# Optimization experiments

Hardware: AMD Instinct MI355X
Metric: run time of the kernel (lower is better)

## Reference

```python
import jax, jax.numpy as jnp
import numpy as np

NUM_HEADS = 16
KEY_DIM = 64
VALUE_DIM = 64
D_MODEL = 1024
NEG_INF = -1e10


def setup_inputs() -> dict:
    key = jax.random.key(0)
    ks = jax.random.split(key, 8)
    B, T, S, D = 4, 2048, 2048, D_MODEL
    w_scale = 1.0 / np.sqrt(D)  # keep logits well-scaled
    inp = {
        'query': jax.random.normal(ks[0], (B, T, D), jnp.float32),
        'key':   jax.random.normal(ks[1], (B, S, D), jnp.float32),
        'value': jax.random.normal(ks[2], (B, S, D), jnp.float32),
        'Wq': jax.random.normal(ks[3], (D, NUM_HEADS * KEY_DIM), jnp.float32) * w_scale,
        'bq': jnp.zeros((NUM_HEADS * KEY_DIM,), jnp.float32),
        'Wk': jax.random.normal(ks[4], (D, NUM_HEADS * KEY_DIM), jnp.float32) * w_scale,
        'bk': jnp.zeros((NUM_HEADS * KEY_DIM,), jnp.float32),
        'Wv': jax.random.normal(ks[5], (D, NUM_HEADS * VALUE_DIM), jnp.float32) * w_scale,
        'bv': jnp.zeros((NUM_HEADS * VALUE_DIM,), jnp.float32),
        'Wo': jax.random.normal(ks[6], (NUM_HEADS * VALUE_DIM, D), jnp.float32) * w_scale,
        'bo': jnp.zeros((D,), jnp.float32),
    }
    return inp


def reference(query, key, value, Wq, bq, Wk, bk, Wv, bv, Wo, bo):
    B, T, _ = query.shape
    S = key.shape[1]
    H, Dk, Dv = NUM_HEADS, KEY_DIM, VALUE_DIM
    # QKV projections -> (B, T/S, H, D_head)
    q = (query @ Wq + bq).reshape(B, T, H, Dk)
    k = (key @ Wk + bk).reshape(B, S, H, Dk)
    v = (value @ Wv + bv).reshape(B, S, H, Dv)
    # scaled dot-product scores: (B, H, T, S)
    q = q * (1.0 / jnp.sqrt(jnp.asarray(Dk, q.dtype)))
    scores = jnp.einsum('bthd,bshd->bhts', q, k)
    # causal mask [1,1,T,S], additive -1e10 on masked positions (as in source)
    causal = jnp.tril(jnp.ones((T, S), scores.dtype))
    scores = scores + NEG_INF * (1.0 - causal)
    attn = jax.nn.softmax(scores, axis=-1)
    # dropout rate = 0.0 -> identity
    ctx = jnp.einsum('bhts,bshd->bthd', attn, v).reshape(B, T, H * Dv)
    out = ctx @ Wo + bo
    return out
```

## Files before the change

kernel.cpp:

```cpp
#include <hip/hip_runtime.h>
#include <cstdint>

#define DEV static __device__ __forceinline__

typedef unsigned short u16;
typedef unsigned int u32;
using short8 = __attribute__((ext_vector_type(8))) short;
using f32x2  = __attribute__((ext_vector_type(2))) float;
using f32x4  = __attribute__((ext_vector_type(4))) float;
using f32x8  = __attribute__((ext_vector_type(8))) float;
using f32x16 = __attribute__((ext_vector_type(16))) float;
using u32x4  = __attribute__((ext_vector_type(4))) unsigned int;

constexpr int Bz = 4, Tz = 2048, Dz = 1024, Hz = 16;
constexpr float QSCALE = 0.125f * 1.4426950408889634f;

DEV u16 f2bf(float x) {
  union { float f; u32 u; } c; c.f = x;
  u32 u = c.u;
  return (u16)((u + 0x7FFFu + ((u >> 16) & 1u)) >> 16);
}

DEV u32 cvtpk(float a, float b) {
  u32 r;
  asm("v_cvt_pk_bf16_f32 %0, %1, %2" : "=v"(r) : "v"(a), "v"(b));
  return r;
}

DEV void gload16(const void* g, void* l) {
  __builtin_amdgcn_global_load_lds(
      (const __attribute__((address_space(1))) void*)g,
      (__attribute__((address_space(3))) void*)l, 16, 0, 0);
}

__global__ __launch_bounds__(256) void cvt_kernel(
    const float* __restrict__ Xq, const float* __restrict__ Xk,
    const float* __restrict__ Xv, u16* __restrict__ Yq,
    u16* __restrict__ Yk, u16* __restrict__ Yv) {
  int z = blockIdx.y;
  const float* X = z == 0 ? Xq : z == 1 ? Xk : Xv;
  u16* Y         = z == 0 ? Yq : z == 1 ? Yk : Yv;
  size_t i = (size_t)blockIdx.x * 256 + threadIdx.x;
  float4 a = ((const float4*)X)[i * 2];
  float4 b = ((const float4*)X)[i * 2 + 1];
  uint4 o;
  o.x = cvtpk(a.x, a.y); o.y = cvtpk(a.z, a.w);
  o.z = cvtpk(b.x, b.y); o.w = cvtpk(b.z, b.w);
  ((uint4*)Y)[i] = o;
}

__global__ void wt_kernel(const float* __restrict__ W0, const float* __restrict__ W1,
                          const float* __restrict__ W2, const float* __restrict__ W3,
                          u16* __restrict__ T0, u16* __restrict__ T1,
                          u16* __restrict__ T2, u16* __restrict__ T3) {
  __shared__ float tile[32][33];
  int z = blockIdx.z;
  const float* W = z == 0 ? W0 : z == 1 ? W1 : z == 2 ? W2 : W3;
  u16* WT = z == 0 ? T0 : z == 1 ? T1 : z == 2 ? T2 : T3;
  int n0 = blockIdx.x * 32, k0 = blockIdx.y * 32;
  int tx = threadIdx.x & 31, ty = threadIdx.x >> 5;
  #pragma unroll
  for (int i = 0; i < 32; i += 8)
    tile[ty + i][tx] = W[(size_t)(k0 + ty + i) * Dz + n0 + tx];
  __syncthreads();
  #pragma unroll
  for (int i = 0; i < 32; i += 8)
    WT[(size_t)(n0 + ty + i) * Dz + k0 + tx] = f2bf(tile[tx][ty + i]);
}

template <int EPI>
DEV void gemm_core(const u16* __restrict__ A, const u16* __restrict__ WT,
                   const float* __restrict__ bias, void* __restrict__ Cptr,
                   float scale, int n0, int m0, char* L)
{
  const int tid = threadIdx.x;
  const int lane = tid & 63, wid = tid >> 6;
  const int g = lane >> 4, l15 = lane & 15;
  const int wm = (wid >> 1) * 64, wn = (wid & 1) * 64;

  f32x4 acc[4][4] = {};

  const int srow = tid >> 3, scolb = (tid & 7) * 16;
  const int scbs = scolb ^ ((srow & 7) << 4);

  for (int step = 0; step < 16; ++step) {
    const int k0 = step * 64;
    #pragma unroll
    for (int i = 0; i < 4; ++i) {
      int row = srow + i * 32;
      gload16(A + (size_t)(m0 + row) * Dz + k0 + (scbs >> 1),
              L + (tid + i * 256) * 16);
    }
    #pragma unroll
    for (int i = 0; i < 4; ++i) {
      int row = srow + i * 32;
      gload16(WT + (size_t)(n0 + row) * Dz + k0 + (scbs >> 1),
              L + 16384 + (tid + i * 256) * 16);
    }
    __syncthreads();

    #pragma unroll
    for (int kc = 0; kc < 2; ++kc) {
      short8 af[4], bfv[4];
      #pragma unroll
      for (int mt = 0; mt < 4; ++mt) {
        int row = wm + mt * 16 + l15;
        af[mt] = *(const short8*)(L + row * 128 + ((kc * 64 + g * 16) ^ ((row & 7) << 4)));
      }
      #pragma unroll
      for (int nt = 0; nt < 4; ++nt) {
        int row = wn + nt * 16 + l15;
        bfv[nt] = *(const short8*)(L + 16384 + row * 128 + ((kc * 64 + g * 16) ^ ((row & 7) << 4)));
      }
      #pragma unroll
      for (int mt = 0; mt < 4; ++mt)
        #pragma unroll
        for (int nt = 0; nt < 4; ++nt)
          acc[mt][nt] = __builtin_amdgcn_mfma_f32_16x16x32_bf16(af[mt], bfv[nt], acc[mt][nt], 0, 0, 0);
    }
    __syncthreads();
  }

  if (EPI == 0) {
    u16* C = (u16*)Cptr;
    #pragma unroll
    for (int nt = 0; nt < 4; ++nt) {
      int n = n0 + wn + nt * 16 + l15;
      float bv = bias[n];
      #pragma unroll
      for (int mt = 0; mt < 4; ++mt)
        #pragma unroll
        for (int r = 0; r < 4; ++r) {
          int m = m0 + wm + mt * 16 + g * 4 + r;
          C[(size_t)m * Dz + n] = f2bf((acc[mt][nt][r] + bv) * scale);
        }
    }
  } else if (EPI == 1) {
    float* C = (float*)Cptr;
    #pragma unroll
    for (int nt = 0; nt < 4; ++nt) {
      int n = n0 + wn + nt * 16 + l15;
      float bv = bias[n];
      #pragma unroll
      for (int mt = 0; mt < 4; ++mt)
        #pragma unroll
        for (int r = 0; r < 4; ++r) {
          int m = m0 + wm + mt * 16 + g * 4 + r;
          C[(size_t)m * Dz + n] = acc[mt][nt][r] + bv;
        }
    }
  } else {
    u16* VT = (u16*)Cptr;
    #pragma unroll
    for (int nt = 0; nt < 4; ++nt) {
      int nrel = wn + nt * 16 + l15;
      float bv = bias[n0 + nrel];
      int swz = (nrel & 7) << 4;
      #pragma unroll
      for (int mt = 0; mt < 4; ++mt) {
        int mrel0 = wm + mt * 16 + g * 4;
        uint2 p = make_uint2(cvtpk(acc[mt][nt][0] + bv, acc[mt][nt][1] + bv),
                             cvtpk(acc[mt][nt][2] + bv, acc[mt][nt][3] + bv));
        *(uint2*)(L + nrel * 256 + ((mrel0 * 2) ^ swz)) = p;
      }
    }
    __syncthreads();
    int n = tid & 127, strip = tid >> 7;
    int nn = n0 + n;
    int h = nn >> 6, dv = nn & 63;
    int b = m0 >> 11;
    int tb = m0 & 2047;
    int swz = (n & 7) << 4;
    u16* dst = VT + (((size_t)(b * Hz + h) * 64 + dv) * Tz) + tb + strip * 64;
    #pragma unroll
    for (int c = 0; c < 8; ++c) {
      uint4 v = *(const uint4*)(L + n * 256 + ((strip * 128 + c * 16) ^ swz));
      *(uint4*)(dst + c * 8) = v;
    }
  }
}

__global__ __launch_bounds__(256, 4) void qkv_kernel(
    const u16* __restrict__ Aq, const u16* __restrict__ Ak, const u16* __restrict__ Av,
    const u16* __restrict__ Wq, const u16* __restrict__ Wk, const u16* __restrict__ Wv,
    const float* __restrict__ bq, const float* __restrict__ bk, const float* __restrict__ bv,
    u16* __restrict__ oq, u16* __restrict__ ok, u16* __restrict__ ovt)
{
  __shared__ char lds[32768];
  int z = blockIdx.z;
  int n0 = blockIdx.y * 128, m0 = blockIdx.x * 128;
  if (z == 0)
    gemm_core<0>(Aq, Wq, bq, oq, QSCALE, n0, m0, lds);
  else if (z == 1)
    gemm_core<0>(Ak, Wk, bk, ok, 1.0f, n0, m0, lds);
  else
    gemm_core<2>(Av, Wv, bv, ovt, 1.0f, n0, m0, lds);
}

__global__ __launch_bounds__(256, 4) void out_gemm_kernel(
    const u16* __restrict__ A, const u16* __restrict__ WT,
    const float* __restrict__ bias, float* __restrict__ C)
{
  __shared__ char lds[32768];
  gemm_core<1>(A, WT, bias, C, 1.0f, blockIdx.y * 128, blockIdx.x * 128, lds);
}

DEV short8 mk_pb(float p0, float p1, float p2, float p3,
                 float p4, float p5, float p6, float p7) {
  u32 x0 = cvtpk(p0, p1), y0 = cvtpk(p4, p5);
  u32 x1 = cvtpk(p2, p3), y1 = cvtpk(p6, p7);
  asm("v_permlane32_swap_b32 %0, %1" : "+v"(x0), "+v"(y0));
  asm("v_permlane32_swap_b32 %0, %1" : "+v"(x1), "+v"(y1));
  u32x4 w = {x0, x1, y0, y1};
  return __builtin_bit_cast(short8, w);
}

DEV float vsum16(f32x16 a, f32x16 b) {
  f32x16 s = a + b;
  f32x8 s8 = __builtin_shufflevector(s, s, 0, 1, 2, 3, 4, 5, 6, 7) +
             __builtin_shufflevector(s, s, 8, 9, 10, 11, 12, 13, 14, 15);
  f32x4 s4 = __builtin_shufflevector(s8, s8, 0, 1, 2, 3) +
             __builtin_shufflevector(s8, s8, 4, 5, 6, 7);
  f32x2 s2 = __builtin_shufflevector(s4, s4, 0, 1) +
             __builtin_shufflevector(s4, s4, 2, 3);
  return s2[0] + s2[1];
}

__global__ __launch_bounds__(512) void attn_kernel(
    const u16* __restrict__ Q, const u16* __restrict__ K,
    const u16* __restrict__ VT, u16* __restrict__ CTX)
{
  __shared__ char lds[65536];

  const int tid = threadIdx.x;
  const int lane = tid & 63, wave = tid >> 6;
  const int s = wave >> 2, w4 = wave & 3;
  const int l31 = lane & 31, hi = lane >> 5;
  const int pr = blockIdx.y;
  const int bh = blockIdx.x;
  const int b = bh >> 4, h = bh & 15;

  const u16* qb  = Q  + (size_t)b * Tz * Dz + h * 64;
  const u16* kb  = K  + (size_t)b * Tz * Dz + h * 64;
  const u16* vtb = VT + (size_t)bh * 64 * Tz;

  #pragma unroll 1
  for (int half = 0; half < 2; ++half) {
    const int j = half ? (15 - pr) : pr;
    const int t0 = j * 128;
    const int nsteps = j + 1;
    const int wq0 = t0 + w4 * 32;
    const int qg = wq0 + l31, wqhi = wq0 + 31;
    const int tbase = s * nsteps;

    auto stage = [&](int buf, int step) {
      #pragma unroll
      for (int i = 0; i < 4; ++i) {
        int c = tid + i * 512;
        int sc = c >> 10, r = c & 1023;
        int tn = r >> 9, e = r & 511;
        int row = e >> 3, colb = (e & 7) * 16;
        int cbs = colb ^ ((row & 7) << 4);
        int kv0 = (sc * nsteps + step) * 64;
        char* dst = lds + ((sc * 2 + buf) << 14) + (tn << 13) + e * 16;
        if (tn == 0)
          gload16(kb + (size_t)(kv0 + row) * Dz + (cbs >> 1), dst);
        else
          gload16(vtb + (size_t)row * Tz + kv0 + (cbs >> 1), dst);
      }
    };

    stage(0, 0);

    short8 qf[4];
    #pragma unroll
    for (int kc = 0; kc < 4; ++kc)
      qf[kc] = *(const short8*)(qb + (size_t)qg * Dz + kc * 16 + hi * 8);

    f32x16 o0 = {}, o1 = {};
    float l_run = 0.f;

    __syncthreads();

    int cur = 0;
    for (int step = 0; step < nsteps; ++step) {
      if (step + 1 < nsteps) stage(cur ^ 1, step + 1);
      const int kv0 = (tbase + step) * 64;

      if (kv0 <= wqhi) {
        const char* Kl = lds + ((s * 2 + cur) << 14);
        const char* Vl = Kl + 8192;
        const int swz = (l31 & 7) << 4;

        f32x16 s0 = {}, s1 = {};
        __builtin_amdgcn_s_setprio(1);
        #pragma unroll
        for (int kc = 0; kc < 4; ++kc) {
          int cb = (kc * 32 + hi * 16) ^ swz;
          short8 kf0 = *(const short8*)(Kl + l31 * 128 + cb);
          short8 kf1 = *(const short8*)(Kl + (32 + l31) * 128 + cb);
          s0 = __builtin_amdgcn_mfma_f32_32x32x16_bf16(kf0, qf[kc], s0, 0, 0, 0);
          s1 = __builtin_amdgcn_mfma_f32_32x32x16_bf16(kf1, qf[kc], s1, 0, 0, 0);
        }
        __builtin_amdgcn_s_setprio(0);

        if (kv0 + 63 > wq0) {
          #pragma unroll
          for (int r = 0; r < 16; ++r) {
            int kg = kv0 + (r & 3) + 8 * (r >> 2) + 4 * hi;
            if (kg > qg)      s0[r] = -3.0e38f;
            if (kg + 32 > qg) s1[r] = -3.0e38f;
          }
        }

        #pragma unroll
        for (int r = 0; r < 16; ++r) {
          s0[r] = __builtin_amdgcn_exp2f(s0[r]);
          s1[r] = __builtin_amdgcn_exp2f(s1[r]);
        }
        float psum = vsum16(s0, s1);
        psum += __shfl_xor(psum, 32);
        l_run += psum;

        short8 pb0 = mk_pb(s0[0], s0[1], s0[2],  s0[3],  s0[4],  s0[5],  s0[6],  s0[7]);
        short8 pb1 = mk_pb(s0[8], s0[9], s0[10], s0[11], s0[12], s0[13], s0[14], s0[15]);
        short8 pb2 = mk_pb(s1[0], s1[1], s1[2],  s1[3],  s1[4],  s1[5],  s1[6],  s1[7]);
        short8 pb3 = mk_pb(s1[8], s1[9], s1[10], s1[11], s1[12], s1[13], s1[14], s1[15]);

        __builtin_amdgcn_s_setprio(1);
        #pragma unroll
        for (int kc = 0; kc < 4; ++kc) {
          int cb = (kc * 32 + hi * 16) ^ swz;
          short8 vf0 = *(const short8*)(Vl + l31 * 128 + cb);
          short8 vf1 = *(const short8*)(Vl + (32 + l31) * 128 + cb);
          short8 pbk = (kc == 0) ? pb0 : (kc == 1) ? pb1 : (kc == 2) ? pb2 : pb3;
          o0 = __builtin_amdgcn_mfma_f32_32x32x16_bf16(vf0, pbk, o0, 0, 0, 0);
          o1 = __builtin_amdgcn_mfma_f32_32x32x16_bf16(vf1, pbk, o1, 0, 0, 0);
        }
        __builtin_amdgcn_s_setprio(0);
      }

      __syncthreads();
      cur ^= 1;
    }

    if (s == 1) {
      char* P = lds + w4 * 9216 + lane * 144;
      #pragma unroll
      for (int r2 = 0; r2 < 4; ++r2) {
        f32x4 a = {o0[4*r2], o0[4*r2+1], o0[4*r2+2], o0[4*r2+3]};
        *(f32x4*)(P + r2 * 16) = a;
        f32x4 c = {o1[4*r2], o1[4*r2+1], o1[4*r2+2], o1[4*r2+3]};
        *(f32x4*)(P + 64 + r2 * 16) = c;
      }
      *(float*)(P + 128) = l_run;
    }
    __syncthreads();
    if (s == 0) {
      const char* P = lds + w4 * 9216 + lane * 144;
      float l1 = *(const float*)(P + 128);
      float inv = 1.0f / (l_run + l1);

      u16* cp = CTX + ((size_t)(b * Tz + qg)) * Dz + h * 64;
      #pragma unroll
      for (int rq = 0; rq < 4; ++rq) {
        f32x4 p0 = *(const f32x4*)(P + rq * 16);
        f32x4 p1 = *(const f32x4*)(P + 64 + rq * 16);
        int dv0 = 8 * rq + 4 * hi;
        float a0 = (o0[rq*4+0] + p0[0]) * inv;
        float a1 = (o0[rq*4+1] + p0[1]) * inv;
        float a2 = (o0[rq*4+2] + p0[2]) * inv;
        float a3 = (o0[rq*4+3] + p0[3]) * inv;
        *(uint2*)(cp + dv0) = make_uint2(cvtpk(a0, a1), cvtpk(a2, a3));
        float c0 = (o1[rq*4+0] + p1[0]) * inv;
        float c1 = (o1[rq*4+1] + p1[1]) * inv;
        float c2 = (o1[rq*4+2] + p1[2]) * inv;
        float c3 = (o1[rq*4+3] + p1[3]) * inv;
        *(uint2*)(cp + 32 + dv0) = make_uint2(cvtpk(c0, c1), cvtpk(c2, c3));
      }
    }
    __syncthreads();
  }
}

extern "C" void kernel_launch(void* const* d_in, const int* in_sizes, int n_in,
                              void* d_out, int out_size, void* d_ws, size_t ws_size,
                              hipStream_t stream) {
  (void)in_sizes; (void)n_in; (void)out_size; (void)ws_size;
  const float* query = (const float*)d_in[0];
  const float* key   = (const float*)d_in[1];
  const float* value = (const float*)d_in[2];
  const float* Wq = (const float*)d_in[3];
  const float* bq = (const float*)d_in[4];
  const float* Wk = (const float*)d_in[5];
  const float* bk = (const float*)d_in[6];
  const float* Wv = (const float*)d_in[7];
  const float* bv = (const float*)d_in[8];
  const float* Wo = (const float*)d_in[9];
  const float* bo = (const float*)d_in[10];

  char* ws = (char*)d_ws;
  const size_t SZ_ACT = (size_t)Bz * Tz * Dz * sizeof(u16);
  const size_t SZ_W = (size_t)Dz * Dz * sizeof(u16);
  u16* qw  = (u16*)(ws);
  u16* kw  = (u16*)(ws + SZ_ACT);
  u16* vw  = (u16*)(ws + 2 * SZ_ACT);
  u16* vtw = (u16*)(ws + 3 * SZ_ACT);
  u16* qx  = vw;
  u16* cw  = vw;
  u16* wqt = (u16*)(ws + 4 * SZ_ACT);
  u16* wkt = (u16*)(ws + 4 * SZ_ACT + SZ_W);
  u16* wvt = (u16*)(ws + 4 * SZ_ACT + 2 * SZ_W);
  u16* wot = (u16*)(ws + 4 * SZ_ACT + 3 * SZ_W);
  u16* kx = (u16*)d_out;
  u16* vx = (u16*)d_out + (size_t)Bz * Tz * Dz;

  const int CVTG = (Bz * Tz * Dz) / (256 * 8);
  cvt_kernel<<<dim3(CVTG, 3), 256, 0, stream>>>(query, key, value, qx, kx, vx);

  wt_kernel<<<dim3(32, 32, 4), 256, 0, stream>>>(Wq, Wk, Wv, Wo, wqt, wkt, wvt, wot);

  qkv_kernel<<<dim3(64, 8, 3), 256, 0, stream>>>(qx, kx, vx,
                                                 wqt, wkt, wvt,
                                                 bq, bk, bv,
                                                 qw, kw, vtw);

  attn_kernel<<<dim3(Bz * Hz, 8), 512, 0, stream>>>(qw, kw, vtw, cw);

  out_gemm_kernel<<<dim3(64, 8), 256, 0, stream>>>(cw, wot, bo, (float*)d_out);
}
```

Before: 171.0 us.

## Fuse fp32-to-bf16 activation conversion into QKV GEMM A-tile loads

Removes the separate conversion kernel and has the QKV GEMM load fp32 activations directly into LDS (with a wider swizzle), converting to bf16 when reading fragments. This drops one full read-write pass over the three activation tensors and a kernel launch. In exchange, each GEMM block reads twice as many A bytes per tile, across all 8 N-tile blocks. LDS use grows to 48KB and occupancy drops from 4 to 3 blocks, and conversion ALU work moves into the MFMA inner loop.

```diff
diff --git a/kernel.cpp b/kernel.cpp
--- a/kernel.cpp
+++ b/kernel.cpp
@@ -31,22 +31,6 @@
   __builtin_amdgcn_global_load_lds(
       (const __attribute__((address_space(1))) void*)g,
       (__attribute__((address_space(3))) void*)l, 16, 0, 0);
-}
-
-__global__ __launch_bounds__(256) void cvt_kernel(
-    const float* __restrict__ Xq, const float* __restrict__ Xk,
-    const float* __restrict__ Xv, u16* __restrict__ Yq,
-    u16* __restrict__ Yk, u16* __restrict__ Yv) {
-  int z = blockIdx.y;
-  const float* X = z == 0 ? Xq : z == 1 ? Xk : Xv;
-  u16* Y         = z == 0 ? Yq : z == 1 ? Yk : Yv;
-  size_t i = (size_t)blockIdx.x * 256 + threadIdx.x;
-  float4 a = ((const float4*)X)[i * 2];
-  float4 b = ((const float4*)X)[i * 2 + 1];
-  uint4 o;
-  o.x = cvtpk(a.x, a.y); o.y = cvtpk(a.z, a.w);
-  o.z = cvtpk(b.x, b.y); o.w = cvtpk(b.z, b.w);
-  ((uint4*)Y)[i] = o;
 }
 
 __global__ void wt_kernel(const float* __restrict__ W0, const float* __restrict__ W1,
@@ -68,11 +52,13 @@
     WT[(size_t)(n0 + ty + i) * Dz + k0 + tx] = f2bf(tile[tx][ty + i]);
 }
 
-template <int EPI>
-DEV void gemm_core(const u16* __restrict__ A, const u16* __restrict__ WT,
+template <int AFP32, int EPI>
+DEV void gemm_core(const void* __restrict__ Aptr, const u16* __restrict__ WT,
                    const float* __restrict__ bias, void* __restrict__ Cptr,
                    float scale, int n0, int m0, char* L)
 {
+  constexpr int BOFF = AFP32 ? 32768 : 16384;
+
   const int tid = threadIdx.x;
   const int lane = tid & 63, wid = tid >> 6;
   const int g = lane >> 4, l15 = lane & 15;
@@ -82,20 +68,33 @@
 
   const int srow = tid >> 3, scolb = (tid & 7) * 16;
   const int scbs = scolb ^ ((srow & 7) << 4);
+  const int frow = tid >> 4, fcolb = (tid & 15) * 16;
+  const int fcbs = fcolb ^ ((frow & 7) << 5);
 
   for (int step = 0; step < 16; ++step) {
     const int k0 = step * 64;
-    #pragma unroll
-    for (int i = 0; i < 4; ++i) {
-      int row = srow + i * 32;
-      gload16(A + (size_t)(m0 + row) * Dz + k0 + (scbs >> 1),
-              L + (tid + i * 256) * 16);
+    if (AFP32) {
+      const float* A = (const float*)Aptr;
+      #pragma unroll
+      for (int i = 0; i < 8; ++i) {
+        int row = frow + i * 16;
+        gload16(A + (size_t)(m0 + row) * Dz + k0 + (fcbs >> 2),
+                L + (tid + i * 256) * 16);
+      }
+    } else {
+      const u16* A = (const u16*)Aptr;
+      #pragma unroll
+      for (int i = 0; i < 4; ++i) {
+        int row = srow + i * 32;
+        gload16(A + (size_t)(m0 + row) * Dz + k0 + (scbs >> 1),
+                L + (tid + i * 256) * 16);
+      }
     }
     #pragma unroll
     for (int i = 0; i < 4; ++i) {
       int row = srow + i * 32;
       gload16(WT + (size_t)(n0 + row) * Dz + k0 + (scbs >> 1),
-              L + 16384 + (tid + i * 256) * 16);
+              L + BOFF + (tid + i * 256) * 16);
     }
     __syncthreads();
 
@@ -105,12 +104,21 @@
       #pragma unroll
       for (int mt = 0; mt < 4; ++mt) {
         int row = wm + mt * 16 + l15;
-        af[mt] = *(const short8*)(L + row * 128 + ((kc * 64 + g * 16) ^ ((row & 7) << 4)));
+        if (AFP32) {
+          const char* p = L + row * 256 + ((kc * 128 + g * 32) ^ ((row & 7) << 5));
+          f32x4 lo = *(const f32x4*)p;
+          f32x4 hi = *(const f32x4*)(p + 16);
+          u32x4 w = {cvtpk(lo[0], lo[1]), cvtpk(lo[2], lo[3]),
+                     cvtpk(hi[0], hi[1]), cvtpk(hi[2], hi[3])};
+          af[mt] = __builtin_bit_cast(short8, w);
+        } else {
+          af[mt] = *(const short8*)(L + row * 128 + ((kc * 64 + g * 16) ^ ((row & 7) << 4)));
+        }
       }
       #pragma unroll
       for (int nt = 0; nt < 4; ++nt) {
         int row = wn + nt * 16 + l15;
-        bfv[nt] = *(const short8*)(L + 16384 + row * 128 + ((kc * 64 + g * 16) ^ ((row & 7) << 4)));
+        bfv[nt] = *(const short8*)(L + BOFF + row * 128 + ((kc * 64 + g * 16) ^ ((row & 7) << 4)));
       }
       #pragma unroll
       for (int mt = 0; mt < 4; ++mt)
@@ -180,21 +188,21 @@
   }
 }
 
-__global__ __launch_bounds__(256, 4) void qkv_kernel(
-    const u16* __restrict__ Aq, const u16* __restrict__ Ak, const u16* __restrict__ Av,
+__global__ __launch_bounds__(256, 3) void qkv_kernel(
+    const float* __restrict__ Aq, const float* __restrict__ Ak, const float* __restrict__ Av,
     const u16* __restrict__ Wq, const u16* __restrict__ Wk, const u16* __restrict__ Wv,
     const float* __restrict__ bq, const float* __restrict__ bk, const float* __restrict__ bv,
     u16* __restrict__ oq, u16* __restrict__ ok, u16* __restrict__ ovt)
 {
-  __shared__ char lds[32768];
+  __shared__ char lds[49152];
   int z = blockIdx.z;
   int n0 = blockIdx.y * 128, m0 = blockIdx.x * 128;
   if (z == 0)
-    gemm_core<0>(Aq, Wq, bq, oq, QSCALE, n0, m0, lds);
+    gemm_core<1, 0>(Aq, Wq, bq, oq, QSCALE, n0, m0, lds);
   else if (z == 1)
-    gemm_core<0>(Ak, Wk, bk, ok, 1.0f, n0, m0, lds);
+    gemm_core<1, 0>(Ak, Wk, bk, ok, 1.0f, n0, m0, lds);
   else
-    gemm_core<2>(Av, Wv, bv, ovt, 1.0f, n0, m0, lds);
+    gemm_core<1, 2>(Av, Wv, bv, ovt, 1.0f, n0, m0, lds);
 }
 
 __global__ __launch_bounds__(256, 4) void out_gemm_kernel(
@@ -202,7 +210,7 @@
     const float* __restrict__ bias, float* __restrict__ C)
 {
   __shared__ char lds[32768];
-  gemm_core<1>(A, WT, bias, C, 1.0f, blockIdx.y * 128, blockIdx.x * 128, lds);
+  gemm_core<0, 1>(A, WT, bias, C, 1.0f, blockIdx.y * 128, blockIdx.x * 128, lds);
 }
 
 DEV short8 mk_pb(float p0, float p1, float p2, float p3,
@@ -404,23 +412,16 @@
   const size_t SZ_W = (size_t)Dz * Dz * sizeof(u16);
   u16* qw  = (u16*)(ws);
   u16* kw  = (u16*)(ws + SZ_ACT);
-  u16* vw  = (u16*)(ws + 2 * SZ_ACT);
+  u16* cw  = (u16*)(ws + 2 * SZ_ACT);
   u16* vtw = (u16*)(ws + 3 * SZ_ACT);
-  u16* qx  = vw;
-  u16* cw  = vw;
   u16* wqt = (u16*)(ws + 4 * SZ_ACT);
   u16* wkt = (u16*)(ws + 4 * SZ_ACT + SZ_W);
   u16* wvt = (u16*)(ws + 4 * SZ_ACT + 2 * SZ_W);
   u16* wot = (u16*)(ws + 4 * SZ_ACT + 3 * SZ_W);
-  u16* kx = (u16*)d_out;
-  u16* vx = (u16*)d_out + (size_t)Bz * Tz * Dz;
-
-  const int CVTG = (Bz * Tz * Dz) / (256 * 8);
-  cvt_kernel<<<dim3(CVTG, 3), 256, 0, stream>>>(query, key, value, qx, kx, vx);
 
   wt_kernel<<<dim3(32, 32, 4), 256, 0, stream>>>(Wq, Wk, Wv, Wo, wqt, wkt, wvt, wot);
 
-  qkv_kernel<<<dim3(64, 8, 3), 256, 0, stream>>>(qx, kx, vx,
+  qkv_kernel<<<dim3(64, 8, 3), 256, 0, stream>>>(query, key, value,
                                                  wqt, wkt, wvt,
                                                  bq, bk, bv,
                                                  qw, kw, vtw);
```

Measured after the change: 163.4 us. -4.5%, faster.

## Enlarge GEMM tiles to 256x128 with 512-thread blocks

Applied to the files above, without the earlier changes.

Doubles the M dimension of the projection GEMM tiles from 128 to 256 and uses 8 waves per block, so each B (weight) tile loaded into LDS is reused across twice as many rows. The V-transpose epilogue is split into two halves to fit the LDS staging buffer. This cuts weight-tile global traffic and halves the grid size, at the cost of fewer blocks (768/256) and more LDS per block, which may lower occupancy or leave the GPU under-filled.

```diff
diff --git a/kernel.cpp b/kernel.cpp
--- a/kernel.cpp
+++ b/kernel.cpp
@@ -73,6 +73,7 @@
                    const float* __restrict__ bias, void* __restrict__ Cptr,
                    float scale, int n0, int m0, char* L)
 {
+  char* Bl = L + 32768;
   const int tid = threadIdx.x;
   const int lane = tid & 63, wid = tid >> 6;
   const int g = lane >> 4, l15 = lane & 15;
@@ -80,22 +81,22 @@
 
   f32x4 acc[4][4] = {};
 
-  const int srow = tid >> 3, scolb = (tid & 7) * 16;
-  const int scbs = scolb ^ ((srow & 7) << 4);
+  const int arow = tid >> 3, colb = (tid & 7) * 16;
+  const int cbs = colb ^ ((arow & 7) << 4);
 
   for (int step = 0; step < 16; ++step) {
     const int k0 = step * 64;
     #pragma unroll
     for (int i = 0; i < 4; ++i) {
-      int row = srow + i * 32;
-      gload16(A + (size_t)(m0 + row) * Dz + k0 + (scbs >> 1),
-              L + (tid + i * 256) * 16);
-    }
-    #pragma unroll
-    for (int i = 0; i < 4; ++i) {
-      int row = srow + i * 32;
-      gload16(WT + (size_t)(n0 + row) * Dz + k0 + (scbs >> 1),
-              L + 16384 + (tid + i * 256) * 16);
+      int row = arow + i * 64;
+      gload16(A + (size_t)(m0 + row) * Dz + k0 + (cbs >> 1),
+              L + (tid + i * 512) * 16);
+    }
+    #pragma unroll
+    for (int i = 0; i < 2; ++i) {
+      int row = arow + i * 64;
+      gload16(WT + (size_t)(n0 + row) * Dz + k0 + (cbs >> 1),
+              Bl + (tid + i * 512) * 16);
     }
     __syncthreads();
 
@@ -110,7 +111,7 @@
       #pragma unroll
       for (int nt = 0; nt < 4; ++nt) {
         int row = wn + nt * 16 + l15;
-        bfv[nt] = *(const short8*)(L + 16384 + row * 128 + ((kc * 64 + g * 16) ^ ((row & 7) << 4)));
+        bfv[nt] = *(const short8*)(Bl + row * 128 + ((kc * 64 + g * 16) ^ ((row & 7) << 4)));
       }
       #pragma unroll
       for (int mt = 0; mt < 4; ++mt)
@@ -151,44 +152,56 @@
     }
   } else {
     u16* VT = (u16*)Cptr;
-    #pragma unroll
-    for (int nt = 0; nt < 4; ++nt) {
-      int nrel = wn + nt * 16 + l15;
-      float bv = bias[n0 + nrel];
-      int swz = (nrel & 7) << 4;
-      #pragma unroll
-      for (int mt = 0; mt < 4; ++mt) {
-        int mrel0 = wm + mt * 16 + g * 4;
-        uint2 p = make_uint2(cvtpk(acc[mt][nt][0] + bv, acc[mt][nt][1] + bv),
-                             cvtpk(acc[mt][nt][2] + bv, acc[mt][nt][3] + bv));
-        *(uint2*)(L + nrel * 256 + ((mrel0 * 2) ^ swz)) = p;
-      }
-    }
-    __syncthreads();
-    int n = tid & 127, strip = tid >> 7;
-    int nn = n0 + n;
-    int h = nn >> 6, dv = nn & 63;
-    int b = m0 >> 11;
-    int tb = m0 & 2047;
-    int swz = (n & 7) << 4;
-    u16* dst = VT + (((size_t)(b * Hz + h) * 64 + dv) * Tz) + tb + strip * 64;
-    #pragma unroll
-    for (int c = 0; c < 8; ++c) {
-      uint4 v = *(const uint4*)(L + n * 256 + ((strip * 128 + c * 16) ^ swz));
-      *(uint4*)(dst + c * 8) = v;
+    const int b = m0 >> 11, tb = m0 & 2047;
+    #pragma unroll 1
+    for (int mh = 0; mh < 2; ++mh) {
+      __syncthreads();
+      if ((wid >> 1) == mh * 2 || (wid >> 1) == mh * 2 + 1) {
+        #pragma unroll
+        for (int nt = 0; nt < 4; ++nt) {
+          int nrel = wn + nt * 16 + l15;
+          float bv = bias[n0 + nrel];
+          int swz = (nrel & 7) << 4;
+          #pragma unroll
+          for (int mt = 0; mt < 4; ++mt) {
+            int mrel0 = wm - mh * 128 + mt * 16 + g * 4;
+            uint2 p = make_uint2(cvtpk(acc[mt][nt][0] + bv, acc[mt][nt][1] + bv),
+                                 cvtpk(acc[mt][nt][2] + bv, acc[mt][nt][3] + bv));
+            *(uint2*)(L + nrel * 256 + ((mrel0 * 2) ^ swz)) = p;
+          }
+        }
+      }
+      __syncthreads();
+      if (tid < 256) {
+        int n = tid & 127, strip = tid >> 7;
+        int nn = n0 + n;
+        int h = nn >> 6, dv = nn & 63;
+        int swz = (n & 7) << 4;
+        u16* dst = VT + (((size_t)(b * Hz + h) * 64 + dv) * Tz) + tb + mh * 128 + strip * 64;
+        #pragma unroll
+        for (int c = 0; c < 4; ++c) {
+          uint4 v = *(const uint4*)(L + n * 256 + ((strip * 128 + c * 16) ^ swz));
+          *(uint4*)(dst + c * 8) = v;
+        }
+        #pragma unroll
+        for (int c = 4; c < 8; ++c) {
+          uint4 v = *(const uint4*)(L + n * 256 + ((strip * 128 + c * 16) ^ swz));
+          *(uint4*)(dst + c * 8) = v;
+        }
+      }
     }
   }
 }
 
-__global__ __launch_bounds__(256, 4) void qkv_kernel(
+__global__ __launch_bounds__(512, 4) void qkv_kernel(
     const u16* __restrict__ Aq, const u16* __restrict__ Ak, const u16* __restrict__ Av,
     const u16* __restrict__ Wq, const u16* __restrict__ Wk, const u16* __restrict__ Wv,
     const float* __restrict__ bq, const float* __restrict__ bk, const float* __restrict__ bv,
     u16* __restrict__ oq, u16* __restrict__ ok, u16* __restrict__ ovt)
 {
-  __shared__ char lds[32768];
+  __shared__ char lds[49152];
   int z = blockIdx.z;
-  int n0 = blockIdx.y * 128, m0 = blockIdx.x * 128;
+  int n0 = blockIdx.y * 128, m0 = blockIdx.x * 256;
   if (z == 0)
     gemm_core<0>(Aq, Wq, bq, oq, QSCALE, n0, m0, lds);
   else if (z == 1)
@@ -197,12 +210,12 @@
     gemm_core<2>(Av, Wv, bv, ovt, 1.0f, n0, m0, lds);
 }
 
-__global__ __launch_bounds__(256, 4) void out_gemm_kernel(
+__global__ __launch_bounds__(512, 4) void out_gemm_kernel(
     const u16* __restrict__ A, const u16* __restrict__ WT,
     const float* __restrict__ bias, float* __restrict__ C)
 {
-  __shared__ char lds[32768];
-  gemm_core<1>(A, WT, bias, C, 1.0f, blockIdx.y * 128, blockIdx.x * 128, lds);
+  __shared__ char lds[49152];
+  gemm_core<1>(A, WT, bias, C, 1.0f, blockIdx.y * 128, blockIdx.x * 256, lds);
 }
 
 DEV short8 mk_pb(float p0, float p1, float p2, float p3,
@@ -404,10 +417,9 @@
   const size_t SZ_W = (size_t)Dz * Dz * sizeof(u16);
   u16* qw  = (u16*)(ws);
   u16* kw  = (u16*)(ws + SZ_ACT);
-  u16* vw  = (u16*)(ws + 2 * SZ_ACT);
+  u16* cw  = (u16*)(ws + 2 * SZ_ACT);
   u16* vtw = (u16*)(ws + 3 * SZ_ACT);
-  u16* qx  = vw;
-  u16* cw  = vw;
+  u16* qx  = cw;
   u16* wqt = (u16*)(ws + 4 * SZ_ACT);
   u16* wkt = (u16*)(ws + 4 * SZ_ACT + SZ_W);
   u16* wvt = (u16*)(ws + 4 * SZ_ACT + 2 * SZ_W);
@@ -420,12 +432,12 @@
 
   wt_kernel<<<dim3(32, 32, 4), 256, 0, stream>>>(Wq, Wk, Wv, Wo, wqt, wkt, wvt, wot);
 
-  qkv_kernel<<<dim3(64, 8, 3), 256, 0, stream>>>(qx, kx, vx,
+  qkv_kernel<<<dim3(32, 8, 3), 512, 0, stream>>>(qx, kx, vx,
                                                  wqt, wkt, wvt,
                                                  bq, bk, bv,
                                                  qw, kw, vtw);
 
   attn_kernel<<<dim3(Bz * Hz, 8), 512, 0, stream>>>(qw, kw, vtw, cw);
 
-  out_gemm_kernel<<<dim3(64, 8), 256, 0, stream>>>(cw, wot, bo, (float*)d_out);
-}
+  out_gemm_kernel<<<dim3(32, 8), 512, 0, stream>>>(cw, wot, bo, (float*)d_out);
+}
```

Result: slower. 189.2 us (+10.7%).
